# Kernel optimization log

Measured on AMD Instinct MI355X. Metric: run time of the kernel, lower is better.

The kernel has to match this reference:

```python
import jax, jax.numpy as jnp
import numpy as np

D_IN = 2048
D_OUT = 2048
NUM_HEADS = 16
NUM_GROUPS = 4
HEAD_DIM = D_OUT // NUM_HEADS          # 128
HEADS_PER_GROUP = NUM_HEADS // NUM_GROUPS  # 4


def setup_inputs() -> dict:
    key = jax.random.key(0)
    ks = jax.random.split(key, 6)
    b, s = 2, 2048
    x = jax.random.normal(ks[0], (b, s, D_IN), dtype=jnp.float32)
    # Store weights as [in, out] so y = x @ W (equivalent to torch Linear x @ W.T)
    sc_q = 1.0 / np.sqrt(D_IN)
    Wq = jax.random.uniform(ks[1], (D_IN, D_OUT), jnp.float32, -sc_q, sc_q)
    Wk = jax.random.uniform(ks[2], (D_IN, NUM_GROUPS * HEAD_DIM), jnp.float32, -sc_q, sc_q)
    Wv = jax.random.uniform(ks[3], (D_IN, NUM_GROUPS * HEAD_DIM), jnp.float32, -sc_q, sc_q)
    sc_o = 1.0 / np.sqrt(D_OUT)
    Wo = jax.random.uniform(ks[4], (D_OUT, D_OUT), jnp.float32, -sc_o, sc_o)
    bo = jax.random.uniform(ks[5], (D_OUT,), jnp.float32, -sc_o, sc_o)
    return {"x": x, "Wq": Wq, "Wk": Wk, "Wv": Wv, "Wo": Wo, "bo": bo}


def reference(x, Wq, Wk, Wv, Wo, bo):
    b, s, _ = x.shape
    g, hpg, hd = NUM_GROUPS, HEADS_PER_GROUP, HEAD_DIM
    # Projections; keep grouped layout instead of repeat_interleave (same math)
    q = (x @ Wq).reshape(b, s, g, hpg, hd)   # query heads ordered group-major,
                                             # matching repeat_interleave of K/V
    k = (x @ Wk).reshape(b, s, g, hd)
    v = (x @ Wv).reshape(b, s, g, hd)
    # scores: [b, g, hpg, q_len, k_len]
    scores = jnp.einsum('bqghd,bkgd->bghqk', q, k)
    causal = jnp.triu(jnp.ones((s, s), dtype=bool), k=1)  # True above diagonal
    scores = jnp.where(causal, -jnp.inf, scores)
    scale = 1.0 / jnp.sqrt(jnp.asarray(hd, dtype=scores.dtype))
    attn = jax.nn.softmax(scores * scale, axis=-1)
    ctx = jnp.einsum('bghqk,bkgd->bqghd', attn, v).reshape(b, s, D_OUT)
    return ctx @ Wo + bo
```

## Files before the change

kernel.cpp:

```cpp
#include <hip/hip_runtime.h>

typedef short v8s __attribute__((ext_vector_type(8)));
typedef float v4f __attribute__((ext_vector_type(4)));

__device__ __forceinline__ short f2bf(float f) {
  union { float f; unsigned u; } v; v.f = f;
  unsigned r = v.u + 0x7FFFu + ((v.u >> 16) & 1u);
  return (short)(r >> 16);
}

__device__ __forceinline__ void gll16(const short* g, short* l) {
  __builtin_amdgcn_global_load_lds(
      (const __attribute__((address_space(1))) void*)g,
      (__attribute__((address_space(3))) void*)l, 16, 0, 0);
}

__global__ void cast_f32_bf16(const float* __restrict__ in, short* __restrict__ out, int n4) {
  int i = blockIdx.x * blockDim.x + threadIdx.x;
  if (i >= n4) return;
  float4 v = ((const float4*)in)[i];
  short4 o;
  o.x = f2bf(v.x); o.y = f2bf(v.y); o.z = f2bf(v.z); o.w = f2bf(v.w);
  ((short4*)out)[i] = o;
}

__global__ void cast_transpose_f32_bf16(const float* __restrict__ in, short* __restrict__ out,
                                        int R, int C) {
  __shared__ float tile[32][33];
  const int tx = threadIdx.x, ty = threadIdx.y;
  const int c0 = blockIdx.x * 32, r0 = blockIdx.y * 32;
#pragma unroll
  for (int i = 0; i < 4; ++i)
    tile[ty + 8 * i][tx] = in[(size_t)(r0 + ty + 8 * i) * C + c0 + tx];
  __syncthreads();
#pragma unroll
  for (int i = 0; i < 4; ++i)
    out[(size_t)(c0 + ty + 8 * i) * R + r0 + tx] = f2bf(tile[tx][ty + 8 * i]);
}

__global__ void transpose_v(const short* __restrict__ qkv, short* __restrict__ out) {
  __shared__ short tile[32][33];
  const int tx = threadIdx.x, ty = threadIdx.y;
  const int c0 = blockIdx.x * 32, r0 = blockIdx.y * 32;
  const int z = blockIdx.z;
#pragma unroll
  for (int i = 0; i < 4; ++i)
    tile[ty + 8 * i][tx] = qkv[(size_t)(z * 2048 + r0 + ty + 8 * i) * 3072 + 2560 + c0 + tx];
  __syncthreads();
#pragma unroll
  for (int i = 0; i < 4; ++i)
    out[(size_t)z * 512 * 2048 + (size_t)(c0 + ty + 8 * i) * 2048 + r0 + tx] = tile[tx][ty + 8 * i];
}

template <int BF16_OUT>
__global__ __launch_bounds__(256) void gemm_bt(const short* __restrict__ A,
                                               const short* __restrict__ Bt,
                                               void* __restrict__ Cout,
                                               const float* __restrict__ bias,
                                               int M, int N, int K) {
  __shared__ short As[128 * 32];
  __shared__ short Bs[128 * 32];
  const int tid = threadIdx.x;
  const int m0 = blockIdx.y * 128, n0 = blockIdx.x * 128;
  const int w = tid >> 6, lane = tid & 63, quad = lane >> 4, l16 = lane & 15;
  const int wm = (w >> 1) * 64, wn = (w & 1) * 64;
  v4f acc[4][4] = {};
  const int srow = lane >> 2, scol = (lane & 3) * 8;
  const short* Ap = A + (size_t)(m0 + w * 32 + srow) * K + scol;
  const short* Bp = Bt + (size_t)(n0 + w * 32 + srow) * K + scol;
  short* AsW = &As[(w * 32) * 32 + lane * 8];
  short* BsW = &Bs[(w * 32) * 32 + lane * 8];
  const size_t rstep = (size_t)16 * K;
  for (int k0 = 0; k0 < K; k0 += 32) {
    __syncthreads();
    gll16(Ap, AsW);
    gll16(Ap + rstep, AsW + 16 * 32);
    gll16(Bp, BsW);
    gll16(Bp + rstep, BsW + 16 * 32);
    __syncthreads();
    Ap += 32; Bp += 32;
    v8s af[4], bf[4];
#pragma unroll
    for (int i = 0; i < 4; ++i) af[i] = *(const v8s*)&As[(wm + i * 16 + l16) * 32 + quad * 8];
#pragma unroll
    for (int i = 0; i < 4; ++i) bf[i] = *(const v8s*)&Bs[(wn + i * 16 + l16) * 32 + quad * 8];
#pragma unroll
    for (int mi = 0; mi < 4; ++mi)
#pragma unroll
      for (int ni = 0; ni < 4; ++ni)
        acc[mi][ni] = __builtin_amdgcn_mfma_f32_16x16x32_bf16(af[mi], bf[ni], acc[mi][ni], 0, 0, 0);
  }
#pragma unroll
  for (int mi = 0; mi < 4; ++mi) {
#pragma unroll
    for (int ni = 0; ni < 4; ++ni) {
      const int col = n0 + wn + ni * 16 + l16;
#pragma unroll
      for (int r = 0; r < 4; ++r) {
        const int row = m0 + wm + mi * 16 + quad * 4 + r;
        if (BF16_OUT) {
          ((short*)Cout)[(size_t)row * N + col] = f2bf(acc[mi][ni][r]);
        } else {
          ((float*)Cout)[(size_t)row * N + col] = acc[mi][ni][r] + bias[col];
        }
      }
    }
  }
}

__global__ __launch_bounds__(256) void flash_attn2(const short* __restrict__ QKV,
                                                   const short* __restrict__ Vtb,
                                                   short* __restrict__ ctx) {
  __shared__ short Ks[64][136];
  __shared__ short Vs[128][72];
  __shared__ short Ps[4][16][72];
  const int tid = threadIdx.x;
  const int w = tid >> 6, lane = tid & 63, quad = lane >> 4, l16 = lane & 15;
  const int bh = blockIdx.y;
  const int b = bh >> 4, h = bh & 15, g = h >> 2;
  const float scale = 0.08838834764831845f;

  const int krow = tid >> 2, kc = (tid & 3) * 32;
  const int vrow = tid >> 1, vc = (tid & 1) * 32;
  const short* Kbase = QKV + 2048 + g * 128;
  const short* Vbase = Vtb + ((size_t)b * 512 + g * 128) * 2048;

#pragma unroll 1
  for (int half = 0; half < 2; ++half) {
    const int qt = half ? (31 - blockIdx.x) : blockIdx.x;
    const int q0 = qt * 64;
    const int qrow = q0 + w * 16;

    v8s aq[4];
    {
      const short* Qp = QKV + (size_t)(b * 2048 + qrow + l16) * 3072 + h * 128 + quad * 8;
#pragma unroll
      for (int kk = 0; kk < 4; ++kk) aq[kk] = *(const v8s*)(Qp + kk * 32);
    }
    v4f o[8] = {};
    float m_i[4] = {-1e30f, -1e30f, -1e30f, -1e30f};
    float l_i[4] = {0.f, 0.f, 0.f, 0.f};

    const int nk = qt + 1;
#pragma unroll 1
    for (int kt = 0; kt < nk; ++kt) {
      const int key0 = kt << 6;
      __syncthreads();
      {
        const short* kp = Kbase + (size_t)(b * 2048 + key0 + krow) * 3072 + kc;
        const short* vp = Vbase + (size_t)vrow * 2048 + key0 + vc;
#pragma unroll
        for (int j = 0; j < 4; ++j) {
          *(v8s*)&Ks[krow][kc + j * 8] = *(const v8s*)(kp + j * 8);
          *(v8s*)&Vs[vrow][vc + j * 8] = *(const v8s*)(vp + j * 8);
        }
      }
      __syncthreads();

      v4f sf[4] = {};
#pragma unroll
      for (int kf = 0; kf < 4; ++kf)
#pragma unroll
        for (int kk = 0; kk < 4; ++kk) {
          v8s kfr = *(const v8s*)&Ks[kf * 16 + l16][kk * 32 + quad * 8];
          sf[kf] = __builtin_amdgcn_mfma_f32_16x16x32_bf16(aq[kk], kfr, sf[kf], 0, 0, 0);
        }

      float mloc[4], p[4][4], rs[4], alpha[4];
      const bool diag = (key0 + 63 > qrow);
#pragma unroll
      for (int r = 0; r < 4; ++r) {
        const int row = qrow + quad * 4 + r;
#pragma unroll
        for (int kf = 0; kf < 4; ++kf) {
          float s = sf[kf][r] * scale;
          if (diag && (key0 + kf * 16 + l16 > row)) s = -1e30f;
          sf[kf][r] = s;
        }
        mloc[r] = fmaxf(fmaxf(sf[0][r], sf[1][r]), fmaxf(sf[2][r], sf[3][r]));
      }
#pragma unroll
      for (int off = 1; off < 16; off <<= 1)
#pragma unroll
        for (int r = 0; r < 4; ++r) mloc[r] = fmaxf(mloc[r], __shfl_xor(mloc[r], off));
#pragma unroll
      for (int r = 0; r < 4; ++r) {
        const float mn = fmaxf(m_i[r], mloc[r]);
        alpha[r] = __expf(m_i[r] - mn);
        m_i[r] = mn;
        rs[r] = 0.f;
#pragma unroll
        for (int kf = 0; kf < 4; ++kf) {
          p[kf][r] = __expf(sf[kf][r] - mn);
          rs[r] += p[kf][r];
        }
      }
#pragma unroll
      for (int off = 1; off < 16; off <<= 1)
#pragma unroll
        for (int r = 0; r < 4; ++r) rs[r] += __shfl_xor(rs[r], off);
#pragma unroll
      for (int r = 0; r < 4; ++r) {
        l_i[r] = l_i[r] * alpha[r] + rs[r];
#pragma unroll
        for (int kf = 0; kf < 4; ++kf)
          Ps[w][quad * 4 + r][kf * 16 + l16] = f2bf(p[kf][r]);
      }
#pragma unroll
      for (int n = 0; n < 8; ++n)
#pragma unroll
        for (int r = 0; r < 4; ++r) o[n][r] *= alpha[r];
      __asm__ __volatile__("s_waitcnt lgkmcnt(0)" ::: "memory");
      v8s pa0 = *(const v8s*)&Ps[w][l16][quad * 8];
      v8s pa1 = *(const v8s*)&Ps[w][l16][32 + quad * 8];
#pragma unroll
      for (int n = 0; n < 8; ++n) {
        v8s vf0 = *(const v8s*)&Vs[n * 16 + l16][quad * 8];
        v8s vf1 = *(const v8s*)&Vs[n * 16 + l16][32 + quad * 8];
        o[n] = __builtin_amdgcn_mfma_f32_16x16x32_bf16(pa0, vf0, o[n], 0, 0, 0);
        o[n] = __builtin_amdgcn_mfma_f32_16x16x32_bf16(pa1, vf1, o[n], 0, 0, 0);
      }
    }
    float inv[4];
#pragma unroll
    for (int r = 0; r < 4; ++r) inv[r] = 1.0f / l_i[r];
#pragma unroll
    for (int n = 0; n < 8; ++n)
#pragma unroll
      for (int r = 0; r < 4; ++r) {
        const int row = qrow + quad * 4 + r;
        ctx[(size_t)(b * 2048 + row) * 2048 + h * 128 + n * 16 + l16] = f2bf(o[n][r] * inv[r]);
      }
  }
}

extern "C" void kernel_launch(void* const* d_in, const int* in_sizes, int n_in,
                              void* d_out, int out_size, void* d_ws, size_t ws_size,
                              hipStream_t stream) {
  const float* x = (const float*)d_in[0];
  const float* Wq = (const float*)d_in[1];
  const float* Wk = (const float*)d_in[2];
  const float* Wv = (const float*)d_in[3];
  const float* Wo = (const float*)d_in[4];
  const float* bo = (const float*)d_in[5];
  float* out = (float*)d_out;
  char* ws = (char*)d_ws;

  short* xb    = (short*)(ws);
  short* ctx   = (short*)(ws);
  short* Wqkvt = (short*)(ws + 16777216);
  short* Wot   = (short*)(ws + 29360128);
  short* QKV   = (short*)(ws + 37748736);
  short* Vtb   = (short*)(ws + 62914560);

  dim3 tb(32, 8);
  cast_f32_bf16<<<8192, 256, 0, stream>>>(x, xb, 2097152);
  cast_transpose_f32_bf16<<<dim3(64, 64), tb, 0, stream>>>(Wq, Wqkvt, 2048, 2048);
  cast_transpose_f32_bf16<<<dim3(16, 64), tb, 0, stream>>>(Wk, Wqkvt + (size_t)2048 * 2048, 2048, 512);
  cast_transpose_f32_bf16<<<dim3(16, 64), tb, 0, stream>>>(Wv, Wqkvt + (size_t)2560 * 2048, 2048, 512);
  cast_transpose_f32_bf16<<<dim3(64, 64), tb, 0, stream>>>(Wo, Wot, 2048, 2048);

  gemm_bt<1><<<dim3(24, 32), 256, 0, stream>>>(xb, Wqkvt, (void*)QKV, nullptr, 4096, 3072, 2048);

  transpose_v<<<dim3(16, 64, 2), tb, 0, stream>>>(QKV, Vtb);

  flash_attn2<<<dim3(16, 32), 256, 0, stream>>>(QKV, Vtb, ctx);

  gemm_bt<0><<<dim3(16, 32), 256, 0, stream>>>(ctx, Wot, (void*)out, bo, 4096, 2048, 2048);
}
```

Baseline: 346.8 us.

## Rewrite attention to keep P in registers, drop max tracking, fuse weight casts

The flash-attention kernel is rebuilt around a transposed score MFMA (K as the A operand), so probabilities land in registers already shaped as the A operand of the PV MFMA. This removes the LDS round trip for P. The online-softmax running max and its shuffle reductions are dropped; exp is applied directly to the scaled scores, and row sums come from an extra MFMA against a ones vector. K/V tiles are loaded with global_load_lds into XOR-swizzled LDS, with V's key order permuted in the transpose kernel to match. Each 128-thread block handles one 64-row query tile instead of a pair. The four weight cast-transpose launches are merged into one. Skipping max subtraction can overflow exp for inputs with large scores.

```diff
diff --git a/kernel.cpp b/kernel.cpp
--- a/kernel.cpp
+++ b/kernel.cpp
@@ -24,21 +24,28 @@
   ((short4*)out)[i] = o;
 }
 
-__global__ void cast_transpose_f32_bf16(const float* __restrict__ in, short* __restrict__ out,
-                                        int R, int C) {
+__global__ void cast_transpose_weights(const float* __restrict__ Wq, const float* __restrict__ Wk,
+                                       const float* __restrict__ Wv, const float* __restrict__ Wo,
+                                       short* __restrict__ Wqkvt, short* __restrict__ Wot) {
   __shared__ float tile[32][33];
   const int tx = threadIdx.x, ty = threadIdx.y;
-  const int c0 = blockIdx.x * 32, r0 = blockIdx.y * 32;
+  int bx = blockIdx.x;
+  const float* src; short* dst; int C, cb;
+  if (bx < 64)      { src = Wq; dst = Wqkvt;                        C = 2048; cb = bx; }
+  else if (bx < 80) { src = Wk; dst = Wqkvt + (size_t)2048 * 2048;  C = 512;  cb = bx - 64; }
+  else if (bx < 96) { src = Wv; dst = Wqkvt + (size_t)2560 * 2048;  C = 512;  cb = bx - 80; }
+  else              { src = Wo; dst = Wot;                          C = 2048; cb = bx - 96; }
+  const int c0 = cb * 32, r0 = blockIdx.y * 32;
 #pragma unroll
   for (int i = 0; i < 4; ++i)
-    tile[ty + 8 * i][tx] = in[(size_t)(r0 + ty + 8 * i) * C + c0 + tx];
+    tile[ty + 8 * i][tx] = src[(size_t)(r0 + ty + 8 * i) * C + c0 + tx];
   __syncthreads();
 #pragma unroll
   for (int i = 0; i < 4; ++i)
-    out[(size_t)(c0 + ty + 8 * i) * R + r0 + tx] = f2bf(tile[tx][ty + 8 * i]);
-}
-
-__global__ void transpose_v(const short* __restrict__ qkv, short* __restrict__ out) {
+    dst[(size_t)(c0 + ty + 8 * i) * 2048 + r0 + tx] = f2bf(tile[tx][ty + 8 * i]);
+}
+
+__global__ void transpose_v_perm(const short* __restrict__ qkv, short* __restrict__ out) {
   __shared__ short tile[32][33];
   const int tx = threadIdx.x, ty = threadIdx.y;
   const int c0 = blockIdx.x * 32, r0 = blockIdx.y * 32;
@@ -48,8 +55,11 @@
     tile[ty + 8 * i][tx] = qkv[(size_t)(z * 2048 + r0 + ty + 8 * i) * 3072 + 2560 + c0 + tx];
   __syncthreads();
 #pragma unroll
-  for (int i = 0; i < 4; ++i)
-    out[(size_t)z * 512 * 2048 + (size_t)(c0 + ty + 8 * i) * 2048 + r0 + tx] = tile[tx][ty + 8 * i];
+  for (int i = 0; i < 4; ++i) {
+    int k = r0 + tx;
+    int pk = (k & ~31) | ((((k >> 2) & 3) * 2 + ((k >> 4) & 1)) * 4) | (k & 3);
+    out[(size_t)z * 512 * 2048 + (size_t)(c0 + ty + 8 * i) * 2048 + pk] = tile[tx][ty + 8 * i];
+  }
 }
 
 template <int BF16_OUT>
@@ -108,128 +118,123 @@
   }
 }
 
-__global__ __launch_bounds__(256) void flash_attn2(const short* __restrict__ QKV,
+__global__ __launch_bounds__(128) void flash_attn3(const short* __restrict__ QKV,
                                                    const short* __restrict__ Vtb,
                                                    short* __restrict__ ctx) {
-  __shared__ short Ks[64][136];
-  __shared__ short Vs[128][72];
-  __shared__ short Ps[4][16][72];
+  __shared__ short Ks[64 * 128];
+  __shared__ short Vs[128 * 64];
   const int tid = threadIdx.x;
   const int w = tid >> 6, lane = tid & 63, quad = lane >> 4, l16 = lane & 15;
+  const int qt = 31 - blockIdx.x;
+  const int q0 = qt * 64;
   const int bh = blockIdx.y;
   const int b = bh >> 4, h = bh & 15, g = h >> 2;
+  const int qb = q0 + w * 32;
   const float scale = 0.08838834764831845f;
 
-  const int krow = tid >> 2, kc = (tid & 3) * 32;
-  const int vrow = tid >> 1, vc = (tid & 1) * 32;
-  const short* Kbase = QKV + 2048 + g * 128;
-  const short* Vbase = Vtb + ((size_t)b * 512 + g * 128) * 2048;
-
+  v8s aq[2][4];
+#pragma unroll
+  for (int qs = 0; qs < 2; ++qs) {
+    const short* Qp = QKV + (size_t)(b * 2048 + qb + qs * 16 + l16) * 3072 + h * 128 + quad * 8;
+#pragma unroll
+    for (int kk = 0; kk < 4; ++kk) aq[qs][kk] = *(const v8s*)(Qp + kk * 32);
+  }
+  v4f o[2][8] = {};
+  v4f ol[2] = {};
+  v8s ones;
+#pragma unroll
+  for (int i = 0; i < 8; ++i) ones[i] = (short)0x3F80;
+
+  const int krbase = w * 32 + (lane >> 4);
+  const int kcl = lane & 15;
+  const short* Kg0 = QKV + (size_t)(b * 2048 + krbase) * 3072 + 2048 + g * 128;
+  const int vrbase = w * 64 + (lane >> 3);
+  const int vcc = ((lane & 7) ^ ((lane >> 3) & 7)) * 8;
+  const short* Vg0 = Vtb + (size_t)(b * 512 + g * 128 + vrbase) * 2048 + vcc;
+
+  const int nk = qt + 1;
 #pragma unroll 1
-  for (int half = 0; half < 2; ++half) {
-    const int qt = half ? (31 - blockIdx.x) : blockIdx.x;
-    const int q0 = qt * 64;
-    const int qrow = q0 + w * 16;
-
-    v8s aq[4];
+  for (int kt = 0; kt < nk; ++kt) {
+    const int key0 = kt << 6;
+    __syncthreads();
     {
-      const short* Qp = QKV + (size_t)(b * 2048 + qrow + l16) * 3072 + h * 128 + quad * 8;
-#pragma unroll
-      for (int kk = 0; kk < 4; ++kk) aq[kk] = *(const v8s*)(Qp + kk * 32);
-    }
-    v4f o[8] = {};
-    float m_i[4] = {-1e30f, -1e30f, -1e30f, -1e30f};
-    float l_i[4] = {0.f, 0.f, 0.f, 0.f};
-
-    const int nk = qt + 1;
-#pragma unroll 1
-    for (int kt = 0; kt < nk; ++kt) {
-      const int key0 = kt << 6;
-      __syncthreads();
-      {
-        const short* kp = Kbase + (size_t)(b * 2048 + key0 + krow) * 3072 + kc;
-        const short* vp = Vbase + (size_t)vrow * 2048 + key0 + vc;
-#pragma unroll
-        for (int j = 0; j < 4; ++j) {
-          *(v8s*)&Ks[krow][kc + j * 8] = *(const v8s*)(kp + j * 8);
-          *(v8s*)&Vs[vrow][vc + j * 8] = *(const v8s*)(vp + j * 8);
+      const short* kg = Kg0 + (size_t)key0 * 3072;
+      const short* vg = Vg0 + key0;
+#pragma unroll
+      for (int ii = 0; ii < 8; ++ii) {
+        const int i = w * 8 + ii;
+        const int c = kcl ^ ((krbase + ii * 4) & 15);
+        gll16(kg + (size_t)(ii * 4) * 3072 + c * 8, &Ks[i * 512 + lane * 8]);
+        gll16(vg + (size_t)(ii * 8) * 2048, &Vs[i * 512 + lane * 8]);
+      }
+    }
+    __syncthreads();
+
+    v4f sf[2][4] = {};
+#pragma unroll
+    for (int kf = 0; kf < 4; ++kf)
+#pragma unroll
+      for (int kk = 0; kk < 4; ++kk) {
+        v8s kfr = *(const v8s*)&Ks[(kf * 16 + l16) * 128 + (((kk * 4 + quad) ^ l16) * 8)];
+        sf[0][kf] = __builtin_amdgcn_mfma_f32_16x16x32_bf16(kfr, aq[0][kk], sf[0][kf], 0, 0, 0);
+        sf[1][kf] = __builtin_amdgcn_mfma_f32_16x16x32_bf16(kfr, aq[1][kk], sf[1][kf], 0, 0, 0);
+      }
+
+    const bool diag = (key0 + 63 > qb);
+    v8s pa[2][2];
+#pragma unroll
+    for (int qs = 0; qs < 2; ++qs) {
+      const int qg = qb + qs * 16 + l16;
+#pragma unroll
+      for (int kf = 0; kf < 4; ++kf)
+#pragma unroll
+        for (int r = 0; r < 4; ++r) {
+          float s = sf[qs][kf][r] * scale;
+          if (diag && (key0 + kf * 16 + quad * 4 + r > qg)) s = -1e30f;
+          sf[qs][kf][r] = __expf(s);
         }
-      }
-      __syncthreads();
-
-      v4f sf[4] = {};
-#pragma unroll
-      for (int kf = 0; kf < 4; ++kf)
-#pragma unroll
-        for (int kk = 0; kk < 4; ++kk) {
-          v8s kfr = *(const v8s*)&Ks[kf * 16 + l16][kk * 32 + quad * 8];
-          sf[kf] = __builtin_amdgcn_mfma_f32_16x16x32_bf16(aq[kk], kfr, sf[kf], 0, 0, 0);
+#pragma unroll
+      for (int hf = 0; hf < 2; ++hf) {
+        v8s t;
+#pragma unroll
+        for (int r = 0; r < 4; ++r) {
+          t[r] = f2bf(sf[qs][hf * 2][r]);
+          t[4 + r] = f2bf(sf[qs][hf * 2 + 1][r]);
         }
-
-      float mloc[4], p[4][4], rs[4], alpha[4];
-      const bool diag = (key0 + 63 > qrow);
+        pa[qs][hf] = t;
+      }
+    }
+
+#pragma unroll
+    for (int nf = 0; nf < 8; ++nf) {
+      const int rowd = nf * 16 + l16;
+      v8s vf0 = *(const v8s*)&Vs[rowd * 64 + ((quad ^ (l16 & 7)) * 8)];
+      v8s vf1 = *(const v8s*)&Vs[rowd * 64 + (((4 + quad) ^ (l16 & 7)) * 8)];
+#pragma unroll
+      for (int qs = 0; qs < 2; ++qs) {
+        o[qs][nf] = __builtin_amdgcn_mfma_f32_16x16x32_bf16(pa[qs][0], vf0, o[qs][nf], 0, 0, 0);
+        o[qs][nf] = __builtin_amdgcn_mfma_f32_16x16x32_bf16(pa[qs][1], vf1, o[qs][nf], 0, 0, 0);
+      }
+    }
+#pragma unroll
+    for (int qs = 0; qs < 2; ++qs) {
+      ol[qs] = __builtin_amdgcn_mfma_f32_16x16x32_bf16(pa[qs][0], ones, ol[qs], 0, 0, 0);
+      ol[qs] = __builtin_amdgcn_mfma_f32_16x16x32_bf16(pa[qs][1], ones, ol[qs], 0, 0, 0);
+    }
+  }
+
+#pragma unroll
+  for (int qs = 0; qs < 2; ++qs) {
+    float inv[4];
+#pragma unroll
+    for (int r = 0; r < 4; ++r) inv[r] = 1.0f / ol[qs][r];
+#pragma unroll
+    for (int nf = 0; nf < 8; ++nf)
 #pragma unroll
       for (int r = 0; r < 4; ++r) {
-        const int row = qrow + quad * 4 + r;
-#pragma unroll
-        for (int kf = 0; kf < 4; ++kf) {
-          float s = sf[kf][r] * scale;
-          if (diag && (key0 + kf * 16 + l16 > row)) s = -1e30f;
-          sf[kf][r] = s;
-        }
-        mloc[r] = fmaxf(fmaxf(sf[0][r], sf[1][r]), fmaxf(sf[2][r], sf[3][r]));
-      }
-#pragma unroll
-      for (int off = 1; off < 16; off <<= 1)
-#pragma unroll
-        for (int r = 0; r < 4; ++r) mloc[r] = fmaxf(mloc[r], __shfl_xor(mloc[r], off));
-#pragma unroll
-      for (int r = 0; r < 4; ++r) {
-        const float mn = fmaxf(m_i[r], mloc[r]);
-        alpha[r] = __expf(m_i[r] - mn);
-        m_i[r] = mn;
-        rs[r] = 0.f;
-#pragma unroll
-        for (int kf = 0; kf < 4; ++kf) {
-          p[kf][r] = __expf(sf[kf][r] - mn);
-          rs[r] += p[kf][r];
-        }
-      }
-#pragma unroll
-      for (int off = 1; off < 16; off <<= 1)
-#pragma unroll
-        for (int r = 0; r < 4; ++r) rs[r] += __shfl_xor(rs[r], off);
-#pragma unroll
-      for (int r = 0; r < 4; ++r) {
-        l_i[r] = l_i[r] * alpha[r] + rs[r];
-#pragma unroll
-        for (int kf = 0; kf < 4; ++kf)
-          Ps[w][quad * 4 + r][kf * 16 + l16] = f2bf(p[kf][r]);
-      }
-#pragma unroll
-      for (int n = 0; n < 8; ++n)
-#pragma unroll
-        for (int r = 0; r < 4; ++r) o[n][r] *= alpha[r];
-      __asm__ __volatile__("s_waitcnt lgkmcnt(0)" ::: "memory");
-      v8s pa0 = *(const v8s*)&Ps[w][l16][quad * 8];
-      v8s pa1 = *(const v8s*)&Ps[w][l16][32 + quad * 8];
-#pragma unroll
-      for (int n = 0; n < 8; ++n) {
-        v8s vf0 = *(const v8s*)&Vs[n * 16 + l16][quad * 8];
-        v8s vf1 = *(const v8s*)&Vs[n * 16 + l16][32 + quad * 8];
-        o[n] = __builtin_amdgcn_mfma_f32_16x16x32_bf16(pa0, vf0, o[n], 0, 0, 0);
-        o[n] = __builtin_amdgcn_mfma_f32_16x16x32_bf16(pa1, vf1, o[n], 0, 0, 0);
-      }
-    }
-    float inv[4];
-#pragma unroll
-    for (int r = 0; r < 4; ++r) inv[r] = 1.0f / l_i[r];
-#pragma unroll
-    for (int n = 0; n < 8; ++n)
-#pragma unroll
-      for (int r = 0; r < 4; ++r) {
-        const int row = qrow + quad * 4 + r;
-        ctx[(size_t)(b * 2048 + row) * 2048 + h * 128 + n * 16 + l16] = f2bf(o[n][r] * inv[r]);
+        const int row = qb + qs * 16 + quad * 4 + r;
+        ctx[(size_t)(b * 2048 + row) * 2048 + h * 128 + nf * 16 + l16] =
+            f2bf(o[qs][nf][r] * inv[r]);
       }
   }
 }
@@ -255,16 +260,13 @@
 
   dim3 tb(32, 8);
   cast_f32_bf16<<<8192, 256, 0, stream>>>(x, xb, 2097152);
-  cast_transpose_f32_bf16<<<dim3(64, 64), tb, 0, stream>>>(Wq, Wqkvt, 2048, 2048);
-  cast_transpose_f32_bf16<<<dim3(16, 64), tb, 0, stream>>>(Wk, Wqkvt + (size_t)2048 * 2048, 2048, 512);
-  cast_transpose_f32_bf16<<<dim3(16, 64), tb, 0, stream>>>(Wv, Wqkvt + (size_t)2560 * 2048, 2048, 512);
-  cast_transpose_f32_bf16<<<dim3(64, 64), tb, 0, stream>>>(Wo, Wot, 2048, 2048);
+  cast_transpose_weights<<<dim3(160, 64), tb, 0, stream>>>(Wq, Wk, Wv, Wo, Wqkvt, Wot);
 
   gemm_bt<1><<<dim3(24, 32), 256, 0, stream>>>(xb, Wqkvt, (void*)QKV, nullptr, 4096, 3072, 2048);
 
-  transpose_v<<<dim3(16, 64, 2), tb, 0, stream>>>(QKV, Vtb);
-
-  flash_attn2<<<dim3(16, 32), 256, 0, stream>>>(QKV, Vtb, ctx);
+  transpose_v_perm<<<dim3(16, 64, 2), tb, 0, stream>>>(QKV, Vtb);
+
+  flash_attn3<<<dim3(32, 32), 128, 0, stream>>>(QKV, Vtb, ctx);
 
   gemm_bt<0><<<dim3(16, 32), 256, 0, stream>>>(ctx, Wot, (void*)out, bo, 4096, 2048, 2048);
 }
```

After: 381.1 us. 1.1x slower.
